# Kernel tuning notes

Measured on AMD Instinct MI355X. Metric: run time of the kernel, lower is better.

Reference implementation:

```python
import jax, jax.numpy as jnp
import numpy as np

B, S, H, D = 32, 512, 768, 64  # batch, seq_len, hidden_size, inner_dim
BIG = 1e12


def _rope(x, sin_pos, cos_pos):
    # x: [B,S,D]; rotate pairs: [-x1, x0, -x3, x2, ...]
    x2 = jnp.stack([-x[..., 1::2], x[..., ::2]], axis=-1).reshape(x.shape)
    return x * cos_pos + x2 * sin_pos


def setup_inputs() -> dict:
    key = jax.random.key(0)
    k1, k2, k3 = jax.random.split(key, 3)
    hidden = jax.random.normal(k1, (B, S, H), dtype=jnp.float32)
    attention_mask = jnp.ones((B, S), dtype=jnp.float32)
    span_ids = jax.random.randint(k2, (B, S, S), 0, 2).astype(jnp.int32)
    dense_w = jax.random.normal(k3, (H, 2 * D), dtype=jnp.float32) * 0.02
    dense_b = jnp.zeros((2 * D,), dtype=jnp.float32)
    return {"hidden": hidden, "attention_mask": attention_mask,
            "span_ids": span_ids, "dense_w": dense_w, "dense_b": dense_b}


def reference(hidden, attention_mask, span_ids, dense_w, dense_b):
    b, s, _ = hidden.shape
    out = hidden @ dense_w + dense_b            # [B,S,2D]
    qw, kw = out[..., :D], out[..., D:]
    # sinusoidal position embedding, interleaved [s0,c0,s1,c1,...]
    pos = jnp.arange(s, dtype=jnp.float32)[:, None]              # [S,1]
    inv_freq = 10000.0 ** (-2.0 * jnp.arange(D // 2, dtype=jnp.float32) / D)
    ang = pos * inv_freq                                         # [S,D/2]
    sin_pos = jnp.repeat(jnp.sin(ang), 2, axis=-1)[None]         # [1,S,D]
    cos_pos = jnp.repeat(jnp.cos(ang), 2, axis=-1)[None]
    qw = _rope(qw, sin_pos, cos_pos)
    kw = _rope(kw, sin_pos, cos_pos)
    logits = jnp.einsum('bmd,bnd->bmn', qw, kw)                  # [B,S,S]
    pad = attention_mask[:, None, :]                             # mask keys (n)
    logits = logits * pad - (1.0 - pad) * BIG
    tril = jnp.tril(jnp.ones((s, s), logits.dtype), -1)          # strict lower
    logits = logits - tril * BIG
    logits = logits / (D ** 0.5)
    # multilabel categorical crossentropy over rows [B*S, S]
    y_true = span_ids.astype(logits.dtype).reshape(b * s, -1)
    y_pred = logits.reshape(b * s, -1)
    yp = (1.0 - 2.0 * y_true) * y_pred
    zeros = jnp.zeros((b * s, 1), yp.dtype)
    y_neg = jnp.concatenate([yp - y_true * BIG, zeros], axis=-1)
    y_pos = jnp.concatenate([yp - (1.0 - y_true) * BIG, zeros], axis=-1)
    loss = (jax.nn.logsumexp(y_neg, axis=-1) + jax.nn.logsumexp(y_pos, axis=-1)).mean()
    return loss
```

## Files before the change

kernel.cpp:

```cpp
#include <hip/hip_runtime.h>
#include <hip/hip_bf16.h>
#include <math.h>

#define Bb   32
#define Ss   512
#define Hh   768
#define Dd   64
#define ND   128
#define Mrows (Bb*Ss)
#define BIGF 1.0e12f

typedef __attribute__((ext_vector_type(8))) short short8;
typedef __attribute__((ext_vector_type(4))) float floatx4;

__device__ __forceinline__ short f2bf(float x) {
    unsigned u = __builtin_bit_cast(unsigned, x);
    u = (u + 0x7FFF + ((u >> 16) & 1)) >> 16;
    return (short)u;
}

__global__ __launch_bounds__(256) void prep_kernel(
    const float* __restrict__ w, short* __restrict__ wfrag,
    float2* __restrict__ rt)
{
    int idx = blockIdx.x * 256 + threadIdx.x;
    int j    = idx & 7;
    int lane = (idx >> 3) & 63;
    int rest = idx >> 9;
    int c    = rest % 24;
    int tt   = rest / 24;
    int n    = tt * 16 + (lane & 15);
    int k    = c * 32 + (lane >> 4) * 8 + j;
    wfrag[idx] = f2bf(w[k * ND + n]);
    if (idx < Ss * 32) {
        int spos = idx >> 5;
        int i    = idx & 31;
        float ln_base = -logf(10000.0f) / 32.0f;
        float invf = expf(ln_base * (float)i);
        float sn, cs;
        sincosf((float)spos * invf, &sn, &cs);
        rt[idx] = make_float2(sn, cs);
    }
}

__global__ __launch_bounds__(256, 2) void proj_rope_kernel(
    const float*  __restrict__ hidden,
    const short*  __restrict__ wfrag,
    const float*  __restrict__ bias,
    const float2* __restrict__ rt,
    short* __restrict__ qbf,
    short* __restrict__ kbf)
{
    const int tid   = threadIdx.x;
    const int w     = tid >> 6;
    const int lane  = tid & 63;
    const int quad  = lane >> 4;
    const int l15   = lane & 15;
    const int h     = w & 1;
    const int mrow0 = blockIdx.x * 32 + (w >> 1) * 16;

    const float* ap  = hidden + (size_t)(mrow0 + l15) * Hh + quad * 8;
    const short* bp0 = wfrag + (size_t)(h * 4) * 24 * 512 + lane * 8;

    floatx4 acc[4] = {{0.f,0.f,0.f,0.f},{0.f,0.f,0.f,0.f},
                      {0.f,0.f,0.f,0.f},{0.f,0.f,0.f,0.f}};

    float4 A0[2], A1[2];
    short8 Bf[2][4];

#define PLOAD(buf, c) do {                                        \
    A0[buf] = *(const float4*)(ap + (c) * 32);                    \
    A1[buf] = *(const float4*)(ap + (c) * 32 + 4);                \
    Bf[buf][0] = *(const short8*)(bp0 + 0 * 24 * 512 + (c) * 512);\
    Bf[buf][1] = *(const short8*)(bp0 + 1 * 24 * 512 + (c) * 512);\
    Bf[buf][2] = *(const short8*)(bp0 + 2 * 24 * 512 + (c) * 512);\
    Bf[buf][3] = *(const short8*)(bp0 + 3 * 24 * 512 + (c) * 512);\
} while (0)

#define PCOMP(buf) do {                                         \
    short8 av;                                                  \
    av[0] = f2bf(A0[buf].x); av[1] = f2bf(A0[buf].y);           \
    av[2] = f2bf(A0[buf].z); av[3] = f2bf(A0[buf].w);           \
    av[4] = f2bf(A1[buf].x); av[5] = f2bf(A1[buf].y);           \
    av[6] = f2bf(A1[buf].z); av[7] = f2bf(A1[buf].w);           \
    acc[0] = __builtin_amdgcn_mfma_f32_16x16x32_bf16(av, Bf[buf][0], acc[0], 0, 0, 0); \
    acc[1] = __builtin_amdgcn_mfma_f32_16x16x32_bf16(av, Bf[buf][1], acc[1], 0, 0, 0); \
    acc[2] = __builtin_amdgcn_mfma_f32_16x16x32_bf16(av, Bf[buf][2], acc[2], 0, 0, 0); \
    acc[3] = __builtin_amdgcn_mfma_f32_16x16x32_bf16(av, Bf[buf][3], acc[3], 0, 0, 0); \
} while (0)

    PLOAD(0, 0);
    #pragma unroll
    for (int cc = 0; cc < 12; ++cc) {
        if (2 * cc + 1 < 24) PLOAD(1, 2 * cc + 1);
        PCOMP(0);
        if (2 * cc + 2 < 24) PLOAD(0, 2 * cc + 2);
        PCOMP(1);
    }
#undef PLOAD
#undef PCOMP

    short* dst = h ? kbf : qbf;
    const float* bptr = bias + h * 64;

    #pragma unroll
    for (int t = 0; t < 4; ++t) {
        const int d  = t * 16 + l15;
        const float bz = bptr[d];
        const float2* rtp = rt + (d >> 1);
        #pragma unroll
        for (int reg = 0; reg < 4; ++reg) {
            const int grow = mrow0 + quad * 4 + reg;
            const int spos = grow & (Ss - 1);
            float2 sc = rtp[spos * 32];
            float x  = acc[t][reg] + bz;
            float xo = __shfl_xor(x, 1);
            float o  = (d & 1) ? (x * sc.y + xo * sc.x)
                               : (x * sc.y - xo * sc.x);
            dst[(size_t)grow * Dd + d] = f2bf(o);
        }
    }
}

__global__ __launch_bounds__(512, 4) void span_loss_kernel(
    const short* __restrict__ qbf,
    const short* __restrict__ kbf,
    const float* __restrict__ mask,
    const int*   __restrict__ span,
    double* __restrict__ rowsum)
{
    const int b    = blockIdx.x >> 4;
    const int m0   = (blockIdx.x & 15) * 32;
    const int tid  = threadIdx.x;
    const int w    = tid >> 6;
    const int lane = tid & 63;
    const int quad = lane >> 4;
    const int l15  = lane & 15;
    const int rh   = w & 1;
    const int cg   = w >> 1;
    const int rbase = m0 + rh * 16;
    const int cbase = cg * 128;

    __shared__ float part[2][4][32];
    __shared__ float bred[2][32];

    int spv[8][4];
    float pdv[8];
    {
        const int* spp = span + ((size_t)(b * Ss + rbase + quad * 4)) * Ss
                              + cbase + l15;
        #pragma unroll
        for (int t = 0; t < 8; ++t) {
            pdv[t] = mask[b * Ss + cbase + t * 16 + l15];
            #pragma unroll
            for (int reg = 0; reg < 4; ++reg)
                spv[t][reg] = spp[(size_t)reg * Ss + t * 16];
        }
    }

    const short* qp = qbf + (size_t)(b * Ss + rbase + l15) * Dd + quad * 8;
    short8 a0 = *(const short8*)(qp);
    short8 a1 = *(const short8*)(qp + 32);

    floatx4 acc[8];
    #pragma unroll
    for (int t = 0; t < 8; ++t) acc[t] = (floatx4){0.f, 0.f, 0.f, 0.f};

    const short* kp = kbf + (size_t)(b * Ss + cbase + l15) * Dd + quad * 8;
    #pragma unroll
    for (int t = 0; t < 8; ++t) {
        short8 bv = *(const short8*)(kp + (size_t)t * 16 * Dd);
        acc[t] = __builtin_amdgcn_mfma_f32_16x16x32_bf16(a0, bv, acc[t], 0, 0, 0);
    }
    #pragma unroll
    for (int t = 0; t < 8; ++t) {
        short8 bv = *(const short8*)(kp + (size_t)t * 16 * Dd + 32);
        acc[t] = __builtin_amdgcn_mfma_f32_16x16x32_bf16(a1, bv, acc[t], 0, 0, 0);
    }

    unsigned spb = 0;
    #pragma unroll
    for (int t = 0; t < 8; ++t) {
        const int n = cbase + t * 16 + l15;
        const float pd = pdv[t];
        #pragma unroll
        for (int reg = 0; reg < 4; ++reg) {
            const int m = rbase + quad * 4 + reg;
            const int sv = spv[t][reg];
            float logit = acc[t][reg] * pd - (1.0f - pd) * BIGF;
            if (n < m) logit -= BIGF;
            logit *= 0.125f;
            float ft = (float)sv;
            acc[t][reg] = (1.0f - 2.0f * ft) * logit;
            spb |= (unsigned)(sv != 0) << (t * 4 + reg);
        }
    }

    float mxn[4] = {0.f, 0.f, 0.f, 0.f};
    float mxp[4] = {0.f, 0.f, 0.f, 0.f};
    #pragma unroll
    for (int t = 0; t < 8; ++t) {
        #pragma unroll
        for (int reg = 0; reg < 4; ++reg) {
            float ft = (float)((spb >> (t * 4 + reg)) & 1u);
            float yp = acc[t][reg];
            mxn[reg] = fmaxf(mxn[reg], yp - ft * BIGF);
            mxp[reg] = fmaxf(mxp[reg], yp - (1.0f - ft) * BIGF);
        }
    }
    #pragma unroll
    for (int off = 1; off < 16; off <<= 1) {
        #pragma unroll
        for (int reg = 0; reg < 4; ++reg) {
            mxn[reg] = fmaxf(mxn[reg], __shfl_xor(mxn[reg], off));
            mxp[reg] = fmaxf(mxp[reg], __shfl_xor(mxp[reg], off));
        }
    }
    if (l15 == 0) {
        #pragma unroll
        for (int reg = 0; reg < 4; ++reg) {
            part[0][cg][rh * 16 + quad * 4 + reg] = mxn[reg];
            part[1][cg][rh * 16 + quad * 4 + reg] = mxp[reg];
        }
    }
    __syncthreads();
    if (tid < 64) {
        int np = tid >> 5, r = tid & 31;
        float mv = fmaxf(fmaxf(part[np][0][r], part[np][1][r]),
                         fmaxf(part[np][2][r], part[np][3][r]));
        bred[np][r] = mv;
    }
    __syncthreads();

    float bmn[4], bmp[4];
    #pragma unroll
    for (int reg = 0; reg < 4; ++reg) {
        bmn[reg] = bred[0][rh * 16 + quad * 4 + reg];
        bmp[reg] = bred[1][rh * 16 + quad * 4 + reg];
    }
    float smn[4] = {0.f, 0.f, 0.f, 0.f};
    float smp[4] = {0.f, 0.f, 0.f, 0.f};
    #pragma unroll
    for (int t = 0; t < 8; ++t) {
        #pragma unroll
        for (int reg = 0; reg < 4; ++reg) {
            float ft = (float)((spb >> (t * 4 + reg)) & 1u);
            float yp = acc[t][reg];
            smn[reg] += __expf(yp - ft * BIGF - bmn[reg]);
            smp[reg] += __expf(yp - (1.0f - ft) * BIGF - bmp[reg]);
        }
    }
    #pragma unroll
    for (int off = 1; off < 16; off <<= 1) {
        #pragma unroll
        for (int reg = 0; reg < 4; ++reg) {
            smn[reg] += __shfl_xor(smn[reg], off);
            smp[reg] += __shfl_xor(smp[reg], off);
        }
    }
    if (l15 == 0) {
        #pragma unroll
        for (int reg = 0; reg < 4; ++reg) {
            part[0][cg][rh * 16 + quad * 4 + reg] = smn[reg];
            part[1][cg][rh * 16 + quad * 4 + reg] = smp[reg];
        }
    }
    __syncthreads();

    if (tid < 32) {
        int r = tid;
        float SN = __expf(-bred[0][r])
                 + part[0][0][r] + part[0][1][r] + part[0][2][r] + part[0][3][r];
        float SP = __expf(-bred[1][r])
                 + part[1][0][r] + part[1][1][r] + part[1][2][r] + part[1][3][r];
        float lse = (bred[0][r] + logf(SN)) + (bred[1][r] + logf(SP));
        rowsum[(size_t)(b * Ss + m0 + r)] = (double)lse;
    }
}

__global__ __launch_bounds__(1024) void final_reduce_kernel(
    const double* __restrict__ rowsum, float* __restrict__ out)
{
    __shared__ double sh[1024];
    const int tid = threadIdx.x;
    double s = 0.0;
    #pragma unroll
    for (int i = 0; i < 16; ++i) s += rowsum[tid + i * 1024];
    sh[tid] = s;
    __syncthreads();
    for (int off = 512; off > 0; off >>= 1) {
        if (tid < off) sh[tid] += sh[tid + off];
        __syncthreads();
    }
    if (tid == 0) out[0] = (float)(sh[0] / (double)Mrows);
}

extern "C" void kernel_launch(void* const* d_in, const int* in_sizes, int n_in,
                              void* d_out, int out_size, void* d_ws, size_t ws_size,
                              hipStream_t stream)
{
    const float* hidden = (const float*)d_in[0];
    const float* mask   = (const float*)d_in[1];
    const int*   span   = (const int*)  d_in[2];
    const float* w      = (const float*)d_in[3];
    const float* bias   = (const float*)d_in[4];
    float* out = (float*)d_out;

    char* p = (char*)d_ws;
    double* rowsum = (double*)p;            p += 131072;
    short*  wfrag  = (short*)p;             p += 196608;
    float2* rt     = (float2*)p;            p += 131072;
    short*  qbf    = (short*)p;             p += (size_t)Mrows * Dd * 2;
    short*  kbf    = (short*)p;

    prep_kernel<<<Hh * ND / 256, 256, 0, stream>>>(w, wfrag, rt);
    proj_rope_kernel<<<Mrows / 32, 256, 0, stream>>>(hidden, wfrag, bias, rt, qbf, kbf);
    span_loss_kernel<<<Bb * 16, 512, 0, stream>>>(qbf, kbf, mask, span, rowsum);
    final_reduce_kernel<<<1, 1024, 0, stream>>>(rowsum, out);
}
```

Baseline: 145.7 us.

## Pack span labels into bitmasks and split projection K across warps

```diff
diff --git a/kernel.cpp b/kernel.cpp
--- a/kernel.cpp
+++ b/kernel.cpp
@@ -43,7 +43,17 @@
     }
 }
 
-__global__ __launch_bounds__(256, 2) void proj_rope_kernel(
+__global__ __launch_bounds__(256) void pack_kernel(
+    const int* __restrict__ span, unsigned* __restrict__ spack)
+{
+    int gid = blockIdx.x * 256 + threadIdx.x;
+    int lane = threadIdx.x & 63;
+    unsigned long long m = __ballot(span[gid] != 0);
+    if ((gid & 31) == 0)
+        spack[gid >> 5] = (unsigned)(m >> (lane & 32));
+}
+
+__global__ __launch_bounds__(512, 4) void proj_rope_kernel(
     const float*  __restrict__ hidden,
     const short*  __restrict__ wfrag,
     const float*  __restrict__ bias,
@@ -56,11 +66,15 @@
     const int lane  = tid & 63;
     const int quad  = lane >> 4;
     const int l15   = lane & 15;
-    const int h     = w & 1;
-    const int mrow0 = blockIdx.x * 32 + (w >> 1) * 16;
-
-    const float* ap  = hidden + (size_t)(mrow0 + l15) * Hh + quad * 8;
-    const short* bp0 = wfrag + (size_t)(h * 4) * 24 * 512 + lane * 8;
+    const int rg    = w & 1;
+    const int h     = (w >> 1) & 1;
+    const int kh    = w >> 2;
+    const int mrow0 = blockIdx.x * 32 + rg * 16;
+
+    const float* ap  = hidden + (size_t)(mrow0 + l15) * Hh + quad * 8
+                              + kh * 12 * 32;
+    const short* bp0 = wfrag + (size_t)(h * 4) * 24 * 512 + lane * 8
+                             + kh * 12 * 512;
 
     floatx4 acc[4] = {{0.f,0.f,0.f,0.f},{0.f,0.f,0.f,0.f},
                       {0.f,0.f,0.f,0.f},{0.f,0.f,0.f,0.f}};
@@ -91,14 +105,32 @@
 
     PLOAD(0, 0);
     #pragma unroll
-    for (int cc = 0; cc < 12; ++cc) {
-        if (2 * cc + 1 < 24) PLOAD(1, 2 * cc + 1);
+    for (int cc = 0; cc < 6; ++cc) {
+        if (2 * cc + 1 < 12) PLOAD(1, 2 * cc + 1);
         PCOMP(0);
-        if (2 * cc + 2 < 24) PLOAD(0, 2 * cc + 2);
+        if (2 * cc + 2 < 12) PLOAD(0, 2 * cc + 2);
         PCOMP(1);
     }
 #undef PLOAD
 #undef PCOMP
+
+    __shared__ float lacc[4][16][64];
+    const int slot = w & 3;
+    if (kh == 1) {
+        #pragma unroll
+        for (int t = 0; t < 4; ++t)
+            #pragma unroll
+            for (int reg = 0; reg < 4; ++reg)
+                lacc[slot][t * 4 + reg][lane] = acc[t][reg];
+    }
+    __syncthreads();
+    if (kh == 1) return;
+
+    #pragma unroll
+    for (int t = 0; t < 4; ++t)
+        #pragma unroll
+        for (int reg = 0; reg < 4; ++reg)
+            acc[t][reg] += lacc[slot][t * 4 + reg][lane];
 
     short* dst = h ? kbf : qbf;
     const float* bptr = bias + h * 64;
@@ -126,7 +158,7 @@
     const short* __restrict__ qbf,
     const short* __restrict__ kbf,
     const float* __restrict__ mask,
-    const int*   __restrict__ span,
+    const unsigned* __restrict__ spack,
     double* __restrict__ rowsum)
 {
     const int b    = blockIdx.x >> 4;
@@ -144,24 +176,25 @@
     __shared__ float part[2][4][32];
     __shared__ float bred[2][32];
 
-    int spv[8][4];
-    float pdv[8];
-    {
-        const int* spp = span + ((size_t)(b * Ss + rbase + quad * 4)) * Ss
-                              + cbase + l15;
-        #pragma unroll
-        for (int t = 0; t < 8; ++t) {
-            pdv[t] = mask[b * Ss + cbase + t * 16 + l15];
-            #pragma unroll
-            for (int reg = 0; reg < 4; ++reg)
-                spv[t][reg] = spp[(size_t)reg * Ss + t * 16];
-        }
-    }
-
     const short* qp = qbf + (size_t)(b * Ss + rbase + l15) * Dd + quad * 8;
     short8 a0 = *(const short8*)(qp);
     short8 a1 = *(const short8*)(qp + 32);
 
+    unsigned spw[4][4];
+    float pdv[8];
+    {
+        const unsigned* spp = spack
+            + (size_t)(b * Ss + rbase + quad * 4) * 16 + cg * 4;
+        #pragma unroll
+        for (int reg = 0; reg < 4; ++reg)
+            #pragma unroll
+            for (int g = 0; g < 4; ++g)
+                spw[reg][g] = spp[reg * 16 + g];
+        #pragma unroll
+        for (int t = 0; t < 8; ++t)
+            pdv[t] = mask[b * Ss + cbase + t * 16 + l15];
+    }
+
     floatx4 acc[8];
     #pragma unroll
     for (int t = 0; t < 8; ++t) acc[t] = (floatx4){0.f, 0.f, 0.f, 0.f};
@@ -183,16 +216,17 @@
     for (int t = 0; t < 8; ++t) {
         const int n = cbase + t * 16 + l15;
         const float pd = pdv[t];
+        const int sh = (t & 1) * 16 + l15;
         #pragma unroll
         for (int reg = 0; reg < 4; ++reg) {
             const int m = rbase + quad * 4 + reg;
-            const int sv = spv[t][reg];
+            unsigned bit = (spw[reg][t >> 1] >> sh) & 1u;
             float logit = acc[t][reg] * pd - (1.0f - pd) * BIGF;
             if (n < m) logit -= BIGF;
             logit *= 0.125f;
-            float ft = (float)sv;
+            float ft = (float)bit;
             acc[t][reg] = (1.0f - 2.0f * ft) * logit;
-            spb |= (unsigned)(sv != 0) << (t * 4 + reg);
+            spb |= bit << (t * 4 + reg);
         }
     }
 
@@ -307,14 +341,16 @@
     float* out = (float*)d_out;
 
     char* p = (char*)d_ws;
-    double* rowsum = (double*)p;            p += 131072;
-    short*  wfrag  = (short*)p;             p += 196608;
-    float2* rt     = (float2*)p;            p += 131072;
-    short*  qbf    = (short*)p;             p += (size_t)Mrows * Dd * 2;
-    short*  kbf    = (short*)p;
+    double*   rowsum = (double*)p;          p += 131072;
+    short*    wfrag  = (short*)p;           p += 196608;
+    float2*   rt     = (float2*)p;          p += 131072;
+    unsigned* spack  = (unsigned*)p;        p += (size_t)Mrows * 16 * 4;
+    short*    qbf    = (short*)p;           p += (size_t)Mrows * Dd * 2;
+    short*    kbf    = (short*)p;
 
     prep_kernel<<<Hh * ND / 256, 256, 0, stream>>>(w, wfrag, rt);
-    proj_rope_kernel<<<Mrows / 32, 256, 0, stream>>>(hidden, wfrag, bias, rt, qbf, kbf);
-    span_loss_kernel<<<Bb * 16, 512, 0, stream>>>(qbf, kbf, mask, span, rowsum);
+    pack_kernel<<<Mrows * Ss / 256, 256, 0, stream>>>(span, spack);
+    proj_rope_kernel<<<Mrows / 32, 512, 0, stream>>>(hidden, wfrag, bias, rt, qbf, kbf);
+    span_loss_kernel<<<Bb * 16, 512, 0, stream>>>(qbf, kbf, mask, spack, rowsum);
     final_reduce_kernel<<<1, 1024, 0, stream>>>(rowsum, out);
 }
```

Result: slower. 152.3 us (+4.5%).

## Split-K projection across waves, fold scale into Q, fuse final reduction

Applied to the files above, without the earlier changes.

```diff
diff --git a/kernel.cpp b/kernel.cpp
--- a/kernel.cpp
+++ b/kernel.cpp
@@ -8,7 +8,8 @@
 #define Dd   64
 #define ND   128
 #define Mrows (Bb*Ss)
-#define BIGF 1.0e12f
+#define BIGF  1.0e12f
+#define BIG8F 1.25e11f
 
 typedef __attribute__((ext_vector_type(8))) short short8;
 typedef __attribute__((ext_vector_type(4))) float floatx4;
@@ -21,15 +22,16 @@
 
 __global__ __launch_bounds__(256) void prep_kernel(
     const float* __restrict__ w, short* __restrict__ wfrag,
-    float2* __restrict__ rt)
+    float2* __restrict__ rt, double* __restrict__ partial,
+    unsigned* __restrict__ cnt)
 {
     int idx = blockIdx.x * 256 + threadIdx.x;
     int j    = idx & 7;
     int lane = (idx >> 3) & 63;
     int rest = idx >> 9;
     int c    = rest % 24;
-    int tt   = rest / 24;
-    int n    = tt * 16 + (lane & 15);
+    int t    = rest / 24;
+    int n    = t * 16 + (lane & 15);
     int k    = c * 32 + (lane >> 4) * 8 + j;
     wfrag[idx] = f2bf(w[k * ND + n]);
     if (idx < Ss * 32) {
@@ -41,9 +43,11 @@
         sincosf((float)spos * invf, &sn, &cs);
         rt[idx] = make_float2(sn, cs);
     }
-}
-
-__global__ __launch_bounds__(256, 2) void proj_rope_kernel(
+    if (idx < 512) partial[idx] = 0.0;
+    if (idx == 512) *cnt = 0u;
+}
+
+__global__ __launch_bounds__(256, 3) void proj_rope_kernel(
     const float*  __restrict__ hidden,
     const short*  __restrict__ wfrag,
     const float*  __restrict__ bias,
@@ -52,61 +56,79 @@
     short* __restrict__ kbf)
 {
     const int tid   = threadIdx.x;
-    const int w     = tid >> 6;
+    const int kh    = tid >> 6;
     const int lane  = tid & 63;
     const int quad  = lane >> 4;
     const int l15   = lane & 15;
-    const int h     = w & 1;
-    const int mrow0 = blockIdx.x * 32 + (w >> 1) * 16;
-
-    const float* ap  = hidden + (size_t)(mrow0 + l15) * Hh + quad * 8;
-    const short* bp0 = wfrag + (size_t)(h * 4) * 24 * 512 + lane * 8;
-
-    floatx4 acc[4] = {{0.f,0.f,0.f,0.f},{0.f,0.f,0.f,0.f},
-                      {0.f,0.f,0.f,0.f},{0.f,0.f,0.f,0.f}};
+    const int mrow0 = blockIdx.x * 16;
+
+    const float* ap  = hidden + (size_t)(mrow0 + l15) * Hh + quad * 8
+                              + kh * 6 * 32;
+    const short* bp0 = wfrag + lane * 8 + kh * 6 * 512;
+
+    floatx4 acc[8];
+    #pragma unroll
+    for (int t = 0; t < 8; ++t) acc[t] = (floatx4){0.f, 0.f, 0.f, 0.f};
 
     float4 A0[2], A1[2];
-    short8 Bf[2][4];
-
-#define PLOAD(buf, c) do {                                        \
-    A0[buf] = *(const float4*)(ap + (c) * 32);                    \
-    A1[buf] = *(const float4*)(ap + (c) * 32 + 4);                \
-    Bf[buf][0] = *(const short8*)(bp0 + 0 * 24 * 512 + (c) * 512);\
-    Bf[buf][1] = *(const short8*)(bp0 + 1 * 24 * 512 + (c) * 512);\
-    Bf[buf][2] = *(const short8*)(bp0 + 2 * 24 * 512 + (c) * 512);\
-    Bf[buf][3] = *(const short8*)(bp0 + 3 * 24 * 512 + (c) * 512);\
+    short8 Bf[2][8];
+
+#define PLOAD(buf, c) do {                                          \
+    A0[buf] = *(const float4*)(ap + (c) * 32);                      \
+    A1[buf] = *(const float4*)(ap + (c) * 32 + 4);                  \
+    _Pragma("unroll")                                               \
+    for (int t = 0; t < 8; ++t)                                     \
+        Bf[buf][t] = *(const short8*)(bp0 + t * 24 * 512 + (c) * 512); \
 } while (0)
 
-#define PCOMP(buf) do {                                         \
-    short8 av;                                                  \
-    av[0] = f2bf(A0[buf].x); av[1] = f2bf(A0[buf].y);           \
-    av[2] = f2bf(A0[buf].z); av[3] = f2bf(A0[buf].w);           \
-    av[4] = f2bf(A1[buf].x); av[5] = f2bf(A1[buf].y);           \
-    av[6] = f2bf(A1[buf].z); av[7] = f2bf(A1[buf].w);           \
-    acc[0] = __builtin_amdgcn_mfma_f32_16x16x32_bf16(av, Bf[buf][0], acc[0], 0, 0, 0); \
-    acc[1] = __builtin_amdgcn_mfma_f32_16x16x32_bf16(av, Bf[buf][1], acc[1], 0, 0, 0); \
-    acc[2] = __builtin_amdgcn_mfma_f32_16x16x32_bf16(av, Bf[buf][2], acc[2], 0, 0, 0); \
-    acc[3] = __builtin_amdgcn_mfma_f32_16x16x32_bf16(av, Bf[buf][3], acc[3], 0, 0, 0); \
+#define PCOMP(buf) do {                                             \
+    short8 av;                                                      \
+    av[0] = f2bf(A0[buf].x); av[1] = f2bf(A0[buf].y);               \
+    av[2] = f2bf(A0[buf].z); av[3] = f2bf(A0[buf].w);               \
+    av[4] = f2bf(A1[buf].x); av[5] = f2bf(A1[buf].y);               \
+    av[6] = f2bf(A1[buf].z); av[7] = f2bf(A1[buf].w);               \
+    _Pragma("unroll")                                               \
+    for (int t = 0; t < 8; ++t)                                     \
+        acc[t] = __builtin_amdgcn_mfma_f32_16x16x32_bf16(           \
+                     av, Bf[buf][t], acc[t], 0, 0, 0);              \
 } while (0)
 
     PLOAD(0, 0);
     #pragma unroll
-    for (int cc = 0; cc < 12; ++cc) {
-        if (2 * cc + 1 < 24) PLOAD(1, 2 * cc + 1);
+    for (int cc = 0; cc < 3; ++cc) {
+        PLOAD(1, 2 * cc + 1);
         PCOMP(0);
-        if (2 * cc + 2 < 24) PLOAD(0, 2 * cc + 2);
+        if (2 * cc + 2 < 6) PLOAD(0, 2 * cc + 2);
         PCOMP(1);
     }
 #undef PLOAD
 #undef PCOMP
 
-    short* dst = h ? kbf : qbf;
-    const float* bptr = bias + h * 64;
-
-    #pragma unroll
-    for (int t = 0; t < 4; ++t) {
-        const int d  = t * 16 + l15;
-        const float bz = bptr[d];
+    __shared__ float lacc[3][32][64];
+    if (kh) {
+        #pragma unroll
+        for (int t = 0; t < 8; ++t)
+            #pragma unroll
+            for (int reg = 0; reg < 4; ++reg)
+                lacc[kh - 1][t * 4 + reg][lane] = acc[t][reg];
+    }
+    __syncthreads();
+    if (kh) return;
+
+    #pragma unroll
+    for (int t = 0; t < 8; ++t)
+        #pragma unroll
+        for (int reg = 0; reg < 4; ++reg)
+            acc[t][reg] += lacc[0][t * 4 + reg][lane]
+                         + lacc[1][t * 4 + reg][lane]
+                         + lacc[2][t * 4 + reg][lane];
+
+    #pragma unroll
+    for (int t = 0; t < 8; ++t) {
+        const int n  = t * 16 + l15;
+        const int d  = n & (Dd - 1);
+        const float bz = bias[n];
+        short* dst = (t < 4) ? qbf : kbf;
         const float2* rtp = rt + (d >> 1);
         #pragma unroll
         for (int reg = 0; reg < 4; ++reg) {
@@ -117,6 +139,7 @@
             float xo = __shfl_xor(x, 1);
             float o  = (d & 1) ? (x * sc.y + xo * sc.x)
                                : (x * sc.y - xo * sc.x);
+            if (t < 4) o *= 0.125f;
             dst[(size_t)grow * Dd + d] = f2bf(o);
         }
     }
@@ -127,7 +150,9 @@
     const short* __restrict__ kbf,
     const float* __restrict__ mask,
     const int*   __restrict__ span,
-    double* __restrict__ rowsum)
+    double* __restrict__ partial,
+    unsigned* __restrict__ cnt,
+    float* __restrict__ out)
 {
     const int b    = blockIdx.x >> 4;
     const int m0   = (blockIdx.x & 15) * 32;
@@ -143,6 +168,7 @@
 
     __shared__ float part[2][4][32];
     __shared__ float bred[2][32];
+    __shared__ int   isLast;
 
     int spv[8][4];
     float pdv[8];
@@ -187,9 +213,8 @@
         for (int reg = 0; reg < 4; ++reg) {
             const int m = rbase + quad * 4 + reg;
             const int sv = spv[t][reg];
-            float logit = acc[t][reg] * pd - (1.0f - pd) * BIGF;
-            if (n < m) logit -= BIGF;
-            logit *= 0.125f;
+            float logit = acc[t][reg] * pd - (1.0f - pd) * BIG8F;
+            if (n < m) logit -= BIG8F;
             float ft = (float)sv;
             acc[t][reg] = (1.0f - 2.0f * ft) * logit;
             spb |= (unsigned)(sv != 0) << (t * 4 + reg);
@@ -267,32 +292,37 @@
     }
     __syncthreads();
 
+    float lse = 0.0f;
     if (tid < 32) {
         int r = tid;
         float SN = __expf(-bred[0][r])
                  + part[0][0][r] + part[0][1][r] + part[0][2][r] + part[0][3][r];
         float SP = __expf(-bred[1][r])
                  + part[1][0][r] + part[1][1][r] + part[1][2][r] + part[1][3][r];
-        float lse = (bred[0][r] + logf(SN)) + (bred[1][r] + logf(SP));
-        rowsum[(size_t)(b * Ss + m0 + r)] = (double)lse;
-    }
-}
-
-__global__ __launch_bounds__(1024) void final_reduce_kernel(
-    const double* __restrict__ rowsum, float* __restrict__ out)
-{
-    __shared__ double sh[1024];
-    const int tid = threadIdx.x;
-    double s = 0.0;
-    #pragma unroll
-    for (int i = 0; i < 16; ++i) s += rowsum[tid + i * 1024];
-    sh[tid] = s;
-    __syncthreads();
-    for (int off = 512; off > 0; off >>= 1) {
-        if (tid < off) sh[tid] += sh[tid + off];
-        __syncthreads();
-    }
-    if (tid == 0) out[0] = (float)(sh[0] / (double)Mrows);
+        lse = (bred[0][r] + logf(SN)) + (bred[1][r] + logf(SP));
+    }
+    if (tid < 64) {
+        double dv = (tid < 32) ? (double)lse : 0.0;
+        #pragma unroll
+        for (int off = 1; off < 32; off <<= 1) dv += __shfl_xor(dv, off);
+        if (tid == 0) {
+            partial[blockIdx.x] = dv;
+            __threadfence();
+            unsigned old = atomicAdd(cnt, 1u);
+            isLast = (old == 511u) ? 1 : 0;
+        }
+    }
+    __syncthreads();
+
+    if (isLast && tid < 64) {
+        double s = 0.0;
+        #pragma unroll
+        for (int i = 0; i < 8; ++i)
+            s += atomicAdd(&partial[tid + i * 64], 0.0);
+        #pragma unroll
+        for (int off = 1; off < 64; off <<= 1) s += __shfl_xor(s, off);
+        if (tid == 0) out[0] = (float)(s / (double)Mrows);
+    }
 }
 
 extern "C" void kernel_launch(void* const* d_in, const int* in_sizes, int n_in,
@@ -307,14 +337,14 @@
     float* out = (float*)d_out;
 
     char* p = (char*)d_ws;
-    double* rowsum = (double*)p;            p += 131072;
-    short*  wfrag  = (short*)p;             p += 196608;
-    float2* rt     = (float2*)p;            p += 131072;
-    short*  qbf    = (short*)p;             p += (size_t)Mrows * Dd * 2;
-    short*  kbf    = (short*)p;
-
-    prep_kernel<<<Hh * ND / 256, 256, 0, stream>>>(w, wfrag, rt);
-    proj_rope_kernel<<<Mrows / 32, 256, 0, stream>>>(hidden, wfrag, bias, rt, qbf, kbf);
-    span_loss_kernel<<<Bb * 16, 512, 0, stream>>>(qbf, kbf, mask, span, rowsum);
-    final_reduce_kernel<<<1, 1024, 0, stream>>>(rowsum, out);
-}
+    double*   partial = (double*)p;
+    unsigned* cnt     = (unsigned*)(p + 4096);
+    short*    wfrag   = (short*)(p + 8192);
+    float2*   rt      = (float2*)(p + 8192 + 196608);
+    short*    qbf     = (short*)(p + 8192 + 196608 + 131072);
+    short*    kbf     = qbf + (size_t)Mrows * Dd;
+
+    prep_kernel<<<Hh * ND / 256, 256, 0, stream>>>(w, wfrag, rt, partial, cnt);
+    proj_rope_kernel<<<Mrows / 16, 256, 0, stream>>>(hidden, wfrag, bias, rt, qbf, kbf);
+    span_loss_kernel<<<Bb * 16, 512, 0, stream>>>(qbf, kbf, mask, span, partial, cnt, out);
+}
```

New measurement: 155.8 us. 1.07x slower.
